# Kernel optimization log

Hardware: AMD Instinct MI355X
Metric: run time of the kernel (lower is better)

The kernel has to match this reference:

```python
import jax, jax.numpy as jnp
import numpy as np
import math

NUM_HEADS = 8
HIDDEN = 128  # per-head dim == model dim (residual stream)
B, S = 4, 2048
LN_EPS = 1e-6
NEG = -1e9


def setup_inputs() -> dict:
    key = jax.random.key(0)
    ks = jax.random.split(key, 7)
    enc = jax.random.normal(ks[0], (B, S, HIDDEN), dtype=jnp.float32)
    mask = jax.random.randint(ks[1], (B, 1, S, S), 0, 2, dtype=jnp.int32)
    sc = 1.0 / math.sqrt(HIDDEN)
    Wq = jax.random.normal(ks[2], (HIDDEN, HIDDEN * NUM_HEADS), dtype=jnp.float32) * sc
    Wk = jax.random.normal(ks[3], (HIDDEN, HIDDEN * NUM_HEADS), dtype=jnp.float32) * sc
    Wv = jax.random.normal(ks[4], (HIDDEN, HIDDEN * NUM_HEADS), dtype=jnp.float32) * sc
    Wo = jax.random.normal(ks[5], (HIDDEN * NUM_HEADS, HIDDEN), dtype=jnp.float32) * sc
    ln_scale = jnp.ones((HIDDEN,), dtype=jnp.float32)
    ln_bias = jnp.zeros((HIDDEN,), dtype=jnp.float32)
    return {"enc": enc, "mask": mask, "Wq": Wq, "Wk": Wk, "Wv": Wv,
            "Wo": Wo, "ln_scale": ln_scale, "ln_bias": ln_bias}


def _layer_norm(x, scale, bias):
    mu = jnp.mean(x, axis=-1, keepdims=True)
    var = jnp.mean(jnp.square(x - mu), axis=-1, keepdims=True)
    return (x - mu) * jax.lax.rsqrt(var + LN_EPS) * scale + bias


def reference(enc, mask, Wq, Wk, Wv, Wo, ln_scale, ln_bias):
    b, s, d = enc.shape
    h = Wq.shape[1] // d
    # projections -> [b, h, s, d]
    def proj(W):
        return jnp.einsum('bsd,de->bse', enc, W).reshape(b, s, h, d).transpose(0, 2, 1, 3)
    Q, K, V = proj(Wq), proj(Wk), proj(Wv)
    scores = jnp.einsum('bhqd,bhkd->bhqk', Q, K) / math.sqrt(d)
    scores = jnp.where(mask == 0, jnp.float32(NEG), scores)
    attn = jax.nn.softmax(scores, axis=-1)  # dropout is identity in eval mode
    out = jnp.einsum('bhqk,bhkd->bhqd', attn, V)
    out = out.transpose(0, 2, 1, 3).reshape(b, s, h * d)
    out = jnp.einsum('bse,ed->bsd', out, Wo)
    out = _layer_norm(out + enc, ln_scale, ln_bias)
    return (out, attn)
```

## Files before the change

kernel.cpp:

```cpp
#include <hip/hip_runtime.h>
#include <hip/hip_bf16.h>
#include <cstdint>
#include <cstddef>

typedef __bf16 bf16;
typedef __bf16 bf16x8 __attribute__((ext_vector_type(8)));
typedef float  f32x4  __attribute__((ext_vector_type(4)));
typedef unsigned int uint32;

#define MFMA16(a, b, c) __builtin_amdgcn_mfma_f32_16x16x32_bf16((a), (b), (c), 0, 0, 0)

static constexpr int Bn = 4, Hn = 8, Sn = 2048, Dn = 128, En = 1024;


__global__ void k_cvt_enc(const float* __restrict__ in, bf16* __restrict__ out) {
    int i = blockIdx.x * 256 + threadIdx.x;
    out[i] = (bf16)in[i];
}

__global__ void k_cvt_w(const float* __restrict__ w, bf16* __restrict__ wt,
                        int dinLog, int doutLog, float scale) {
    int idx = blockIdx.x * 256 + threadIdx.x;
    int n = idx >> dinLog;
    int k = idx & ((1 << dinLog) - 1);
    wt[idx] = (bf16)(w[(k << doutLog) + n] * scale);
}

__global__ void k_bitmask(const int* __restrict__ m, uint32* __restrict__ bits) {
    int idx = blockIdx.x * 256 + threadIdx.x;
    unsigned long long b = __ballot(m[idx] != 0);
    if ((threadIdx.x & 63) == 0) {
        bits[(idx >> 5)]     = (uint32)b;
        bits[(idx >> 5) + 1] = (uint32)(b >> 32);
    }
}


__global__ __launch_bounds__(256) void k_proj(const bf16* __restrict__ encB,
                                              const bf16* __restrict__ wT0,
                                              const bf16* __restrict__ wT1,
                                              const bf16* __restrict__ wT2,
                                              bf16* __restrict__ qb,
                                              bf16* __restrict__ kbuf,
                                              bf16* __restrict__ vt) {
    const int tid = threadIdx.x, w = tid >> 6, lane = tid & 63;
    const int quad = lane >> 4, l15 = lane & 15;
    const int mat = blockIdx.z;
    const int hh  = blockIdx.y;
    const int e0  = hh * 128;
    const int row0 = blockIdx.x * 64 + w * 16;
    const bf16* wT = (mat == 0) ? wT0 : ((mat == 1) ? wT1 : wT2);

    bf16x8 a[4];
#pragma unroll
    for (int kc = 0; kc < 4; kc++)
        a[kc] = *(const bf16x8*)(encB + (row0 + l15) * Dn + kc * 32 + quad * 8);

    f32x4 acc[8];
#pragma unroll
    for (int nt = 0; nt < 8; nt++) { f32x4 z = {0.f, 0.f, 0.f, 0.f}; acc[nt] = z; }

#pragma unroll
    for (int kc = 0; kc < 4; kc++) {
#pragma unroll
        for (int nt = 0; nt < 8; nt++) {
            bf16x8 b = *(const bf16x8*)(wT + (e0 + nt * 16 + l15) * Dn + kc * 32 + quad * 8);
            acc[nt] = MFMA16(a[kc], b, acc[nt]);
        }
    }

    __shared__ bf16 tile[4 * 16 * 128];
#pragma unroll
    for (int nt = 0; nt < 8; nt++)
#pragma unroll
        for (int r = 0; r < 4; r++)
            tile[(w * 16 + quad * 4 + r) * 128 + nt * 16 + l15] = (bf16)acc[nt][r];
    __syncthreads();

    if (mat < 2) {
        bf16* outp = (mat == 0) ? qb : kbuf;
#pragma unroll
        for (int it = 0; it < 4; it++) {
            int rr = it * 4 + quad;
            int s  = blockIdx.x * 64 + w * 16 + rr;
            int bb = s >> 11, sl = s & 2047;
            bf16* dst = outp + (((size_t)(bb * Hn + hh) * Sn + sl) * Dn) + l15 * 8;
            *(uint4*)dst = *(const uint4*)(tile + (w * 16 + rr) * 128 + l15 * 8);
        }
    } else {
        int dr  = tid >> 1;
        int sc0 = (tid & 1) * 32;
        int sg  = blockIdx.x * 64;
        int bb  = sg >> 11, sl0 = sg & 2047;
        unsigned short tmp[32];
#pragma unroll
        for (int i = 0; i < 32; i++) {
            int sl = sc0 + i;
            tmp[i] = *(const unsigned short*)(tile + sl * 128 + dr);
        }
        bf16* dst = vt + ((size_t)(bb * Hn + hh) * Dn + dr) * Sn + sl0 + sc0;
#pragma unroll
        for (int i = 0; i < 4; i++)
            *(uint4*)(dst + i * 8) = *(const uint4*)(tmp + i * 8);
    }
}


__global__ __launch_bounds__(256, 2) void k_attn(const bf16* __restrict__ qb,
                                                 const bf16* __restrict__ kbuf,
                                                 const bf16* __restrict__ vt,
                                                 const uint32* __restrict__ bits,
                                                 float* __restrict__ attn,
                                                 bf16* __restrict__ ob) {
    const int tid = threadIdx.x, w = tid >> 6, lane = tid & 63;
    const int quad = lane >> 4, l15 = lane & 15;
    const int qblk = blockIdx.x;
    const int bh   = blockIdx.y;
    const int bb   = bh >> 3, hh = bh & 7;
    const int qw0  = qblk * 128 + w * 32;

    __shared__ __align__(16) char smem[32768];
    float* Pw = (float*)(smem + w * 8192);

    const bf16* Kbase = kbuf + (size_t)bh * Sn * Dn;
    const bf16* Qbase = qb   + (size_t)bh * Sn * Dn;
    const bf16* Vbase = vt   + (size_t)bh * Dn * Sn;
    const uint32* mbase = bits + (size_t)bb * (Sn * (Sn / 32));
    float* attnbase = attn + (size_t)bh * Sn * Sn;

    bf16x8 aq[2][4];
#pragma unroll
    for (int qs = 0; qs < 2; qs++)
#pragma unroll
        for (int kc = 0; kc < 4; kc++)
            aq[qs][kc] = *(const bf16x8*)(Qbase + (qw0 + qs * 16 + l15) * Dn + kc * 32 + quad * 8);

    float lsum[8];
#pragma unroll
    for (int ri = 0; ri < 8; ri++) lsum[ri] = 0.f;

    for (int kb = 0; kb < Sn / 64; kb++) {
        uint32 mw0[8], mw1[8];
#pragma unroll
        for (int ri = 0; ri < 8; ri++) {
            int q = qw0 + (ri >> 2) * 16 + quad * 4 + (ri & 3);
            uint2 m = *(const uint2*)(mbase + (size_t)q * (Sn / 32) + kb * 2);
            mw0[ri] = m.x; mw1[ri] = m.y;
        }

#pragma unroll
        for (int ct = 0; ct < 4; ct++) {
            f32x4 z = {0.f, 0.f, 0.f, 0.f};
            f32x4 sc0 = z, sc1 = z;
            __builtin_amdgcn_s_setprio(1);
#pragma unroll
            for (int kc = 0; kc < 4; kc++) {
                bf16x8 bk = *(const bf16x8*)(Kbase + (size_t)(kb * 64 + ct * 16 + l15) * Dn + kc * 32 + quad * 8);
                sc0 = MFMA16(aq[0][kc], bk, sc0);
                sc1 = MFMA16(aq[1][kc], bk, sc1);
            }
            __builtin_amdgcn_s_setprio(0);
            int sh = (ct & 1) * 16 + l15;
            int hi = ct >> 1;
#pragma unroll
            for (int r = 0; r < 4; r++) {
                uint32 m0 = hi ? mw1[r] : mw0[r];
                float v0 = ((m0 >> sh) & 1u) ? sc0[r] : -1e9f;
                lsum[r] += __expf(v0);
                uint32 m1 = hi ? mw1[4 + r] : mw0[4 + r];
                float v1 = ((m1 >> sh) & 1u) ? sc1[r] : -1e9f;
                lsum[4 + r] += __expf(v1);
            }
        }
    }

    float invl[8];
#pragma unroll
    for (int ri = 0; ri < 8; ri++) {
        float t = lsum[ri];
        t += __shfl_xor(t, 1, 64);
        t += __shfl_xor(t, 2, 64);
        t += __shfl_xor(t, 4, 64);
        t += __shfl_xor(t, 8, 64);
        invl[ri] = (t > 0.f) ? (1.0f / t) : 0.0f;
    }

    f32x4 o[2][8];
#pragma unroll
    for (int qs = 0; qs < 2; qs++)
#pragma unroll
        for (int nt = 0; nt < 8; nt++) { f32x4 z = {0.f, 0.f, 0.f, 0.f}; o[qs][nt] = z; }

    for (int kb = 0; kb < Sn / 64; kb++) {
        uint32 mw0[8], mw1[8];
#pragma unroll
        for (int ri = 0; ri < 8; ri++) {
            int q = qw0 + (ri >> 2) * 16 + quad * 4 + (ri & 3);
            uint2 m = *(const uint2*)(mbase + (size_t)q * (Sn / 32) + kb * 2);
            mw0[ri] = m.x; mw1[ri] = m.y;
        }

#pragma unroll
        for (int kt = 0; kt < 2; kt++) {
#pragma unroll
            for (int ct2 = 0; ct2 < 2; ct2++) {
                int ct = kt * 2 + ct2;
                f32x4 z = {0.f, 0.f, 0.f, 0.f};
                f32x4 s0 = z, s1 = z;
                __builtin_amdgcn_s_setprio(1);
#pragma unroll
                for (int kc = 0; kc < 4; kc++) {
                    bf16x8 bk = *(const bf16x8*)(Kbase + (size_t)(kb * 64 + ct * 16 + l15) * Dn + kc * 32 + quad * 8);
                    s0 = MFMA16(aq[0][kc], bk, s0);
                    s1 = MFMA16(aq[1][kc], bk, s1);
                }
                __builtin_amdgcn_s_setprio(0);
                int sh = (ct & 1) * 16 + l15;
                int hi = ct >> 1;
#pragma unroll
                for (int r = 0; r < 4; r++) {
                    {
                        uint32 m = hi ? mw1[r] : mw0[r];
                        float v = ((m >> sh) & 1u) ? s0[r] : -1e9f;
                        float il = invl[r];
                        float p = __expf(v) * il + ((il == 0.f) ? (1.0f / 2048.0f) : 0.f);
                        Pw[(quad * 4 + r) * 36 + ct2 * 16 + l15] = p;
                    }
                    {
                        uint32 m = hi ? mw1[4 + r] : mw0[4 + r];
                        float v = ((m >> sh) & 1u) ? s1[r] : -1e9f;
                        float il = invl[4 + r];
                        float p = __expf(v) * il + ((il == 0.f) ? (1.0f / 2048.0f) : 0.f);
                        Pw[(16 + quad * 4 + r) * 36 + ct2 * 16 + l15] = p;
                    }
                }
            }
            bf16x8 ap[2];
#pragma unroll
            for (int qs = 0; qs < 2; qs++) {
                f32x4 p0 = *(const f32x4*)(Pw + (qs * 16 + l15) * 36 + quad * 8);
                f32x4 p1 = *(const f32x4*)(Pw + (qs * 16 + l15) * 36 + quad * 8 + 4);
                float* gd = attnbase + (size_t)(qw0 + qs * 16 + l15) * Sn + kb * 64 + kt * 32 + quad * 8;
                __builtin_nontemporal_store(p0, (f32x4*)gd);
                __builtin_nontemporal_store(p1, (f32x4*)(gd + 4));
                bf16x8 t;
                t[0] = (bf16)p0[0]; t[1] = (bf16)p0[1]; t[2] = (bf16)p0[2]; t[3] = (bf16)p0[3];
                t[4] = (bf16)p1[0]; t[5] = (bf16)p1[1]; t[6] = (bf16)p1[2]; t[7] = (bf16)p1[3];
                ap[qs] = t;
            }
            __builtin_amdgcn_s_setprio(1);
#pragma unroll
            for (int nt = 0; nt < 8; nt++) {
                bf16x8 bv = *(const bf16x8*)(Vbase + (size_t)(nt * 16 + l15) * Sn + kb * 64 + kt * 32 + quad * 8);
                o[0][nt] = MFMA16(ap[0], bv, o[0][nt]);
                o[1][nt] = MFMA16(ap[1], bv, o[1][nt]);
            }
            __builtin_amdgcn_s_setprio(0);
        }
    }

    bf16* Ow = (bf16*)(smem + w * 8192);
#pragma unroll
    for (int qs = 0; qs < 2; qs++)
#pragma unroll
        for (int nt = 0; nt < 8; nt++)
#pragma unroll
            for (int r = 0; r < 4; r++)
                Ow[(qs * 16 + quad * 4 + r) * 128 + nt * 16 + l15] = (bf16)o[qs][nt][r];
#pragma unroll
    for (int it = 0; it < 8; it++) {
        int rr = it * 4 + quad;
        int s = qblk * 128 + w * 32 + rr;
        bf16* dst = ob + ((size_t)bb * Sn + s) * En + hh * Dn + l15 * 8;
        *(uint4*)dst = *(const uint4*)(Ow + rr * 128 + l15 * 8);
    }
}


__global__ __launch_bounds__(256) void k_final(const bf16* __restrict__ ob,
                                               const bf16* __restrict__ woT,
                                               const float* __restrict__ enc,
                                               const float* __restrict__ lnsc,
                                               const float* __restrict__ lnbi,
                                               float* __restrict__ out) {
    const int tid = threadIdx.x, w = tid >> 6, lane = tid & 63;
    const int quad = lane >> 4, l15 = lane & 15;
    const int row0 = blockIdx.x * 64 + w * 16;

    f32x4 acc[8];
#pragma unroll
    for (int nt = 0; nt < 8; nt++) { f32x4 z = {0.f, 0.f, 0.f, 0.f}; acc[nt] = z; }

    for (int kc = 0; kc < 32; kc++) {
        bf16x8 a = *(const bf16x8*)(ob + (size_t)(row0 + l15) * En + kc * 32 + quad * 8);
#pragma unroll
        for (int nt = 0; nt < 8; nt++) {
            bf16x8 b = *(const bf16x8*)(woT + (size_t)(nt * 16 + l15) * En + kc * 32 + quad * 8);
            acc[nt] = MFMA16(a, b, acc[nt]);
        }
    }

#pragma unroll
    for (int r = 0; r < 4; r++) {
        int row = row0 + quad * 4 + r;
        float xv[8];
        float s1 = 0.f, s2 = 0.f;
#pragma unroll
        for (int nt = 0; nt < 8; nt++) {
            float xx = acc[nt][r] + enc[(size_t)row * Dn + nt * 16 + l15];
            xv[nt] = xx;
            s1 += xx;
            s2 += xx * xx;
        }
        s1 += __shfl_xor(s1, 1, 64); s2 += __shfl_xor(s2, 1, 64);
        s1 += __shfl_xor(s1, 2, 64); s2 += __shfl_xor(s2, 2, 64);
        s1 += __shfl_xor(s1, 4, 64); s2 += __shfl_xor(s2, 4, 64);
        s1 += __shfl_xor(s1, 8, 64); s2 += __shfl_xor(s2, 8, 64);
        float mu = s1 * (1.0f / 128.0f);
        float var = s2 * (1.0f / 128.0f) - mu * mu;
        float rs = rsqrtf(var + 1e-6f);
#pragma unroll
        for (int nt = 0; nt < 8; nt++) {
            int col = nt * 16 + l15;
            out[(size_t)row * Dn + col] = (xv[nt] - mu) * rs * lnsc[col] + lnbi[col];
        }
    }
}


extern "C" void kernel_launch(void* const* d_in, const int* in_sizes, int n_in,
                              void* d_out, int out_size, void* d_ws, size_t ws_size,
                              hipStream_t stream) {
    (void)in_sizes; (void)n_in; (void)out_size; (void)ws_size;
    const float* enc  = (const float*)d_in[0];
    const int*   mask = (const int*)d_in[1];
    const float* Wq   = (const float*)d_in[2];
    const float* Wk   = (const float*)d_in[3];
    const float* Wv   = (const float*)d_in[4];
    const float* Wo   = (const float*)d_in[5];
    const float* lnsc = (const float*)d_in[6];
    const float* lnbi = (const float*)d_in[7];

    char* ws = (char*)d_ws;
    bf16*   encB = (bf16*)(ws + 0);
    bf16*   WqT  = (bf16*)(ws + 2097152);
    bf16*   WkT  = (bf16*)(ws + 2359296);
    bf16*   WvT  = (bf16*)(ws + 2621440);
    bf16*   WoT  = (bf16*)(ws + 2883584);
    uint32* bits = (uint32*)(ws + 3145728);
    bf16*   QB   = (bf16*)(ws + 5242880);
    bf16*   KB   = (bf16*)(ws + 22020096);
    bf16*   VT   = (bf16*)(ws + 38797312);
    bf16*   OB   = (bf16*)(ws + 55574528);

    float* outp = (float*)d_out;
    float* attn = outp + (size_t)Bn * Sn * Dn;

    k_cvt_enc<<<dim3(4096), dim3(256), 0, stream>>>(enc, encB);
    k_cvt_w<<<dim3(512), dim3(256), 0, stream>>>(Wq, WqT, 7, 10, 0.08838834764831845f);
    k_cvt_w<<<dim3(512), dim3(256), 0, stream>>>(Wk, WkT, 7, 10, 1.0f);
    k_cvt_w<<<dim3(512), dim3(256), 0, stream>>>(Wv, WvT, 7, 10, 1.0f);
    k_cvt_w<<<dim3(512), dim3(256), 0, stream>>>(Wo, WoT, 10, 7, 1.0f);
    k_bitmask<<<dim3(65536), dim3(256), 0, stream>>>(mask, bits);
    k_proj<<<dim3(128, 8, 3), dim3(256), 0, stream>>>(encB, WqT, WkT, WvT, QB, KB, VT);
    k_attn<<<dim3(16, 32), dim3(256), 0, stream>>>(QB, KB, VT, bits, attn, OB);
    k_final<<<dim3(128), dim3(256), 0, stream>>>(OB, WoT, enc, lnsc, lnbi, outp);
}
```

Before: 1.047 ms.

## Stage K and V tiles in shared memory and use eight waves per attention block

The attention kernel now loads each 64-key tile of K (and V in the second pass) cooperatively into padded shared memory, and all waves read their MFMA operands from there instead of from global memory. Blocks grow to 512 threads with 16 query rows per wave instead of 32, which halves per-wave register use so more waves can be resident. This cuts redundant global K/V traffic across waves. The cost is two block-wide barriers per key tile and a larger shared-memory footprint, which could limit how many blocks fit per CU.

```diff
diff --git a/kernel.cpp b/kernel.cpp
--- a/kernel.cpp
+++ b/kernel.cpp
@@ -106,7 +106,7 @@
 }
 
 
-__global__ __launch_bounds__(256, 2) void k_attn(const bf16* __restrict__ qb,
+__global__ __launch_bounds__(512, 4) void k_attn(const bf16* __restrict__ qb,
                                                  const bf16* __restrict__ kbuf,
                                                  const bf16* __restrict__ vt,
                                                  const uint32* __restrict__ bits,
@@ -117,10 +117,13 @@
     const int qblk = blockIdx.x;
     const int bh   = blockIdx.y;
     const int bb   = bh >> 3, hh = bh & 7;
-    const int qw0  = qblk * 128 + w * 32;
-
-    __shared__ __align__(16) char smem[32768];
-    float* Pw = (float*)(smem + w * 8192);
+    const int qw0  = qblk * 128 + w * 16;
+
+    __shared__ __align__(16) char smem[58368];
+    bf16*  Klds = (bf16*)smem;
+    bf16*  Vlds = (bf16*)(smem + 17408);
+    float* Plds = (float*)(smem + 39936);
+    float* Pw   = Plds + w * (16 * 36);
 
     const bf16* Kbase = kbuf + (size_t)bh * Sn * Dn;
     const bf16* Qbase = qb   + (size_t)bh * Sn * Dn;
@@ -128,36 +131,44 @@
     const uint32* mbase = bits + (size_t)bb * (Sn * (Sn / 32));
     float* attnbase = attn + (size_t)bh * Sn * Sn;
 
-    bf16x8 aq[2][4];
-#pragma unroll
-    for (int qs = 0; qs < 2; qs++)
-#pragma unroll
-        for (int kc = 0; kc < 4; kc++)
-            aq[qs][kc] = *(const bf16x8*)(Qbase + (qw0 + qs * 16 + l15) * Dn + kc * 32 + quad * 8);
-
-    float lsum[8];
-#pragma unroll
-    for (int ri = 0; ri < 8; ri++) lsum[ri] = 0.f;
+    const int krow = tid >> 3, kc0 = (tid & 7) * 16;
+    const int vdr  = tid >> 2, vc0 = (tid & 3) * 16;
+
+    bf16x8 aq[4];
+#pragma unroll
+    for (int kc = 0; kc < 4; kc++)
+        aq[kc] = *(const bf16x8*)(Qbase + (qw0 + l15) * Dn + kc * 32 + quad * 8);
+
+    float lsum[4];
+#pragma unroll
+    for (int ri = 0; ri < 4; ri++) lsum[ri] = 0.f;
 
     for (int kb = 0; kb < Sn / 64; kb++) {
-        uint32 mw0[8], mw1[8];
-#pragma unroll
-        for (int ri = 0; ri < 8; ri++) {
-            int q = qw0 + (ri >> 2) * 16 + quad * 4 + (ri & 3);
+        {
+            const bf16* src = Kbase + (size_t)(kb * 64 + krow) * Dn + kc0;
+            bf16* dst = Klds + krow * 136 + kc0;
+            *(uint4*)dst       = *(const uint4*)src;
+            *(uint4*)(dst + 8) = *(const uint4*)(src + 8);
+        }
+        __syncthreads();
+
+        uint32 mw0[4], mw1[4];
+#pragma unroll
+        for (int r = 0; r < 4; r++) {
+            int q = qw0 + quad * 4 + r;
             uint2 m = *(const uint2*)(mbase + (size_t)q * (Sn / 32) + kb * 2);
-            mw0[ri] = m.x; mw1[ri] = m.y;
+            mw0[r] = m.x; mw1[r] = m.y;
         }
 
 #pragma unroll
         for (int ct = 0; ct < 4; ct++) {
             f32x4 z = {0.f, 0.f, 0.f, 0.f};
-            f32x4 sc0 = z, sc1 = z;
+            f32x4 sc0 = z;
             __builtin_amdgcn_s_setprio(1);
 #pragma unroll
             for (int kc = 0; kc < 4; kc++) {
-                bf16x8 bk = *(const bf16x8*)(Kbase + (size_t)(kb * 64 + ct * 16 + l15) * Dn + kc * 32 + quad * 8);
-                sc0 = MFMA16(aq[0][kc], bk, sc0);
-                sc1 = MFMA16(aq[1][kc], bk, sc1);
+                bf16x8 bk = *(const bf16x8*)(Klds + (ct * 16 + l15) * 136 + kc * 32 + quad * 8);
+                sc0 = MFMA16(aq[kc], bk, sc0);
             }
             __builtin_amdgcn_s_setprio(0);
             int sh = (ct & 1) * 16 + l15;
@@ -167,16 +178,14 @@
                 uint32 m0 = hi ? mw1[r] : mw0[r];
                 float v0 = ((m0 >> sh) & 1u) ? sc0[r] : -1e9f;
                 lsum[r] += __expf(v0);
-                uint32 m1 = hi ? mw1[4 + r] : mw0[4 + r];
-                float v1 = ((m1 >> sh) & 1u) ? sc1[r] : -1e9f;
-                lsum[4 + r] += __expf(v1);
             }
         }
-    }
-
-    float invl[8];
-#pragma unroll
-    for (int ri = 0; ri < 8; ri++) {
+        __syncthreads();
+    }
+
+    float invl[4];
+#pragma unroll
+    for (int ri = 0; ri < 4; ri++) {
         float t = lsum[ri];
         t += __shfl_xor(t, 1, 64);
         t += __shfl_xor(t, 2, 64);
@@ -185,19 +194,31 @@
         invl[ri] = (t > 0.f) ? (1.0f / t) : 0.0f;
     }
 
-    f32x4 o[2][8];
-#pragma unroll
-    for (int qs = 0; qs < 2; qs++)
-#pragma unroll
-        for (int nt = 0; nt < 8; nt++) { f32x4 z = {0.f, 0.f, 0.f, 0.f}; o[qs][nt] = z; }
+    f32x4 o[8];
+#pragma unroll
+    for (int nt = 0; nt < 8; nt++) { f32x4 z = {0.f, 0.f, 0.f, 0.f}; o[nt] = z; }
 
     for (int kb = 0; kb < Sn / 64; kb++) {
-        uint32 mw0[8], mw1[8];
-#pragma unroll
-        for (int ri = 0; ri < 8; ri++) {
-            int q = qw0 + (ri >> 2) * 16 + quad * 4 + (ri & 3);
+        {
+            const bf16* src = Kbase + (size_t)(kb * 64 + krow) * Dn + kc0;
+            bf16* dst = Klds + krow * 136 + kc0;
+            *(uint4*)dst       = *(const uint4*)src;
+            *(uint4*)(dst + 8) = *(const uint4*)(src + 8);
+        }
+        {
+            const bf16* src = Vbase + (size_t)vdr * Sn + kb * 64 + vc0;
+            bf16* dst = Vlds + vdr * 88 + vc0;
+            *(uint4*)dst       = *(const uint4*)src;
+            *(uint4*)(dst + 8) = *(const uint4*)(src + 8);
+        }
+        __syncthreads();
+
+        uint32 mw0[4], mw1[4];
+#pragma unroll
+        for (int r = 0; r < 4; r++) {
+            int q = qw0 + quad * 4 + r;
             uint2 m = *(const uint2*)(mbase + (size_t)q * (Sn / 32) + kb * 2);
-            mw0[ri] = m.x; mw1[ri] = m.y;
+            mw0[r] = m.x; mw1[r] = m.y;
         }
 
 #pragma unroll
@@ -206,71 +227,54 @@
             for (int ct2 = 0; ct2 < 2; ct2++) {
                 int ct = kt * 2 + ct2;
                 f32x4 z = {0.f, 0.f, 0.f, 0.f};
-                f32x4 s0 = z, s1 = z;
+                f32x4 s0 = z;
                 __builtin_amdgcn_s_setprio(1);
 #pragma unroll
                 for (int kc = 0; kc < 4; kc++) {
-                    bf16x8 bk = *(const bf16x8*)(Kbase + (size_t)(kb * 64 + ct * 16 + l15) * Dn + kc * 32 + quad * 8);
-                    s0 = MFMA16(aq[0][kc], bk, s0);
-                    s1 = MFMA16(aq[1][kc], bk, s1);
+                    bf16x8 bk = *(const bf16x8*)(Klds + (ct * 16 + l15) * 136 + kc * 32 + quad * 8);
+                    s0 = MFMA16(aq[kc], bk, s0);
                 }
                 __builtin_amdgcn_s_setprio(0);
                 int sh = (ct & 1) * 16 + l15;
                 int hi = ct >> 1;
 #pragma unroll
                 for (int r = 0; r < 4; r++) {
-                    {
-                        uint32 m = hi ? mw1[r] : mw0[r];
-                        float v = ((m >> sh) & 1u) ? s0[r] : -1e9f;
-                        float il = invl[r];
-                        float p = __expf(v) * il + ((il == 0.f) ? (1.0f / 2048.0f) : 0.f);
-                        Pw[(quad * 4 + r) * 36 + ct2 * 16 + l15] = p;
-                    }
-                    {
-                        uint32 m = hi ? mw1[4 + r] : mw0[4 + r];
-                        float v = ((m >> sh) & 1u) ? s1[r] : -1e9f;
-                        float il = invl[4 + r];
-                        float p = __expf(v) * il + ((il == 0.f) ? (1.0f / 2048.0f) : 0.f);
-                        Pw[(16 + quad * 4 + r) * 36 + ct2 * 16 + l15] = p;
-                    }
+                    uint32 m = hi ? mw1[r] : mw0[r];
+                    float v = ((m >> sh) & 1u) ? s0[r] : -1e9f;
+                    float il = invl[r];
+                    float p = __expf(v) * il + ((il == 0.f) ? (1.0f / 2048.0f) : 0.f);
+                    Pw[(quad * 4 + r) * 36 + ct2 * 16 + l15] = p;
                 }
             }
-            bf16x8 ap[2];
-#pragma unroll
-            for (int qs = 0; qs < 2; qs++) {
-                f32x4 p0 = *(const f32x4*)(Pw + (qs * 16 + l15) * 36 + quad * 8);
-                f32x4 p1 = *(const f32x4*)(Pw + (qs * 16 + l15) * 36 + quad * 8 + 4);
-                float* gd = attnbase + (size_t)(qw0 + qs * 16 + l15) * Sn + kb * 64 + kt * 32 + quad * 8;
-                __builtin_nontemporal_store(p0, (f32x4*)gd);
-                __builtin_nontemporal_store(p1, (f32x4*)(gd + 4));
-                bf16x8 t;
-                t[0] = (bf16)p0[0]; t[1] = (bf16)p0[1]; t[2] = (bf16)p0[2]; t[3] = (bf16)p0[3];
-                t[4] = (bf16)p1[0]; t[5] = (bf16)p1[1]; t[6] = (bf16)p1[2]; t[7] = (bf16)p1[3];
-                ap[qs] = t;
-            }
+            f32x4 p0 = *(const f32x4*)(Pw + l15 * 36 + quad * 8);
+            f32x4 p1 = *(const f32x4*)(Pw + l15 * 36 + quad * 8 + 4);
+            float* gd = attnbase + (size_t)(qw0 + l15) * Sn + kb * 64 + kt * 32 + quad * 8;
+            __builtin_nontemporal_store(p0, (f32x4*)gd);
+            __builtin_nontemporal_store(p1, (f32x4*)(gd + 4));
+            bf16x8 ap;
+            ap[0] = (bf16)p0[0]; ap[1] = (bf16)p0[1]; ap[2] = (bf16)p0[2]; ap[3] = (bf16)p0[3];
+            ap[4] = (bf16)p1[0]; ap[5] = (bf16)p1[1]; ap[6] = (bf16)p1[2]; ap[7] = (bf16)p1[3];
             __builtin_amdgcn_s_setprio(1);
 #pragma unroll
             for (int nt = 0; nt < 8; nt++) {
-                bf16x8 bv = *(const bf16x8*)(Vbase + (size_t)(nt * 16 + l15) * Sn + kb * 64 + kt * 32 + quad * 8);
-                o[0][nt] = MFMA16(ap[0], bv, o[0][nt]);
-                o[1][nt] = MFMA16(ap[1], bv, o[1][nt]);
+                bf16x8 bv = *(const bf16x8*)(Vlds + (nt * 16 + l15) * 88 + kt * 32 + quad * 8);
+                o[nt] = MFMA16(ap, bv, o[nt]);
             }
             __builtin_amdgcn_s_setprio(0);
         }
-    }
-
-    bf16* Ow = (bf16*)(smem + w * 8192);
-#pragma unroll
-    for (int qs = 0; qs < 2; qs++)
-#pragma unroll
-        for (int nt = 0; nt < 8; nt++)
-#pragma unroll
-            for (int r = 0; r < 4; r++)
-                Ow[(qs * 16 + quad * 4 + r) * 128 + nt * 16 + l15] = (bf16)o[qs][nt][r];
-#pragma unroll
-    for (int it = 0; it < 8; it++) {
+        __syncthreads();
+    }
+
+    bf16* Ow = (bf16*)(smem + w * 4096);
+#pragma unroll
+    for (int nt = 0; nt < 8; nt++)
+#pragma unroll
+        for (int r = 0; r < 4; r++)
+            Ow[(quad * 4 + r) * 128 + nt * 16 + l15] = (bf16)o[nt][r];
+#pragma unroll
+    for (int it = 0; it < 4; it++) {
         int rr = it * 4 + quad;
-        int s = qblk * 128 + w * 32 + rr;
+        int s = qblk * 128 + w * 16 + rr;
         bf16* dst = ob + ((size_t)bb * Sn + s) * En + hh * Dn + l15 * 8;
         *(uint4*)dst = *(const uint4*)(Ow + rr * 128 + l15 * 8);
     }
@@ -363,6 +367,6 @@
     k_cvt_w<<<dim3(512), dim3(256), 0, stream>>>(Wo, WoT, 10, 7, 1.0f);
     k_bitmask<<<dim3(65536), dim3(256), 0, stream>>>(mask, bits);
     k_proj<<<dim3(128, 8, 3), dim3(256), 0, stream>>>(encB, WqT, WkT, WvT, QB, KB, VT);
-    k_attn<<<dim3(16, 32), dim3(256), 0, stream>>>(QB, KB, VT, bits, attn, OB);
+    k_attn<<<dim3(16, 32), dim3(512), 0, stream>>>(QB, KB, VT, bits, attn, OB);
     k_final<<<dim3(128), dim3(256), 0, stream>>>(OB, WoT, enc, lnsc, lnbi, outp);
 }
```

Measured after the change: 982.4 us. 6.1% less time.
